# Optimization experiments

Measured on AMD Instinct MI355X. Metric: run time of the kernel, lower is better.

Reference implementation:

```python
import jax, jax.numpy as jnp
import numpy as np

N = 4096  # output_size
B = 4096  # batch rows
NEG_SLOPE = 0.02


def setup_inputs() -> dict:
    key = jax.random.key(0)
    k1, k2, k3, k4 = jax.random.split(key, 4)
    x = jax.random.normal(k1, (B, N), dtype=jnp.float32)
    W = jax.random.normal(k2, (N, N), dtype=jnp.float32)        # self.weights
    beta = jax.random.normal(k3, (1,), dtype=jnp.float32)       # self.beta (scalar param)
    beta_res = jax.random.normal(k4, (N,), dtype=jnp.float32)   # self.res.beta
    return {"x": x, "W": W, "beta": beta, "beta_res": beta_res}


def reference(x, W, beta, beta_res):
    # wrho = x.unsqueeze(1) * W.expand(B,-1,-1); row_sum = wrho.sum(2)  ==  x @ W.T
    row_sum = jnp.einsum("bj,ij->bi", x, W)                 # [B, N]
    out = jax.nn.relu(1.0 - beta + row_sum)                 # hlogic(1 - beta + row_sum)
    # ResEventually: relu(1 - (beta_res - (x + out))), then LeakyReLU(0.02)
    res = jax.nn.relu(1.0 - (beta_res - (x + out)))
    return jnp.where(res >= 0, res, NEG_SLOPE * res)
```

## Files before the change

### kernel.cpp

```cpp
#include <hip/hip_runtime.h>


#define NDIM 4096

typedef __bf16 bf16x8 __attribute__((ext_vector_type(8)));
typedef float f32x4 __attribute__((ext_vector_type(4)));

__device__ unsigned short f2bf(float f) {
    unsigned int x;
    __builtin_memcpy(&x, &f, 4);
    unsigned int r = x + 0x7FFFu + ((x >> 16) & 1u);
    return (unsigned short)(r >> 16);
}

__device__ unsigned int pack_bf2(float lo, float hi) {
    return (unsigned int)f2bf(lo) | ((unsigned int)f2bf(hi) << 16);
}

__device__ inline void gload16(const uint4* g, unsigned int* l) {
    __builtin_amdgcn_global_load_lds(
        (const __attribute__((address_space(1))) unsigned int*)g,
        (__attribute__((address_space(3))) unsigned int*)l,
        16, 0, 0);
}

__global__ void convert_f32_bf16_kernel(const float* src, unsigned int* dst) {
    const size_t i = ((size_t)blockIdx.x * blockDim.x + threadIdx.x) * 8;
    float4 v0 = *(const float4*)(src + i);
    float4 v1 = *(const float4*)(src + i + 4);
    uint4 u;
    u.x = pack_bf2(v0.x, v0.y);
    u.y = pack_bf2(v0.z, v0.w);
    u.z = pack_bf2(v1.x, v1.y);
    u.w = pack_bf2(v1.z, v1.w);
    *(uint4*)(dst + i / 2) = u;
}

#define BAR()   __builtin_amdgcn_s_barrier()
#define VMCNT(n) asm volatile("s_waitcnt vmcnt(" #n ")" ::: "memory")
#define PRIO(x) __builtin_amdgcn_s_setprio(x)

#define STAGE_A(buf, h, S) do { \
    gload16(Ab4 + (offA[2*(h)]   + (S)*8), &sAU[buf][(2*(h))*2048   + wq]); \
    gload16(Ab4 + (offA[2*(h)+1] + (S)*8), &sAU[buf][(2*(h)+1)*2048 + wq]); \
} while (0)
#define STAGE_B(buf, h, S) do { \
    gload16(Bb4 + (offB[2*(h)]   + (S)*8), &sBU[buf][(2*(h))*2048   + wq]); \
    gload16(Bb4 + (offB[2*(h)+1] + (S)*8), &sBU[buf][(2*(h)+1)*2048 + wq]); \
} while (0)

#define READ_A4(dst, pbuf, mt0) do { \
    _Pragma("unroll") for (int _m = 0; _m < 4; _m++) { \
        dst[_m][0] = (pbuf)[afB + ((mt0) + _m) * 128]; \
        dst[_m][1] = (pbuf)[afB + ((mt0) + _m) * 128 + 64]; } \
} while (0)
#define READ_B2(dst, pbuf, nt0) do { \
    _Pragma("unroll") for (int _n = 0; _n < 2; _n++) { \
        dst[_n][0] = (pbuf)[bfB + ((nt0) + _n) * 128]; \
        dst[_n][1] = (pbuf)[bfB + ((nt0) + _n) * 128 + 64]; } \
} while (0)

#define MM16(afr, bfr, mt0, nt0) do { \
    _Pragma("unroll") for (int _k = 0; _k < 2; _k++) \
    _Pragma("unroll") for (int _m = 0; _m < 4; _m++) \
    _Pragma("unroll") for (int _n = 0; _n < 2; _n++) \
        acc[(mt0)+_m][(nt0)+_n] = __builtin_amdgcn_mfma_f32_16x16x32_bf16( \
            afr[_m][_k], bfr[_n][_k], acc[(mt0)+_m][(nt0)+_n], 0, 0, 0); \
} while (0)

__global__ void __launch_bounds__(512, 2)
ResFCEventuallyLayer_82205674045459_kernel(
    const unsigned int* Xbf, const unsigned int* Wbf,
    const float* X, const float* Bp, const float* Br,
    float* out)
{
    __shared__ __align__(16) unsigned int sAU[2][8192];
    __shared__ __align__(16) unsigned int sBU[2][8192];

    const int t    = threadIdx.x;
    const int lane = t & 63;
    const int wave = t >> 6;
    const int quad = lane >> 4;
    const int l16  = lane & 15;
    const int wm   = wave >> 2;
    const int wn   = wave & 3;
    const int wq   = wave * 256;

    const int bid = blockIdx.x;
    const int swz = ((bid & 7) << 5) | (bid >> 3);
    const int bm0 = (swz >> 4) * 256;
    const int bn0 = (swz & 15) * 256;

    const uint4* Ab4 = (const uint4*)Xbf;
    const uint4* Bb4 = (const uint4*)Wbf;

    int offA[4], offB[4];
#pragma unroll
    for (int rr = 0; rr < 4; rr++) {
        const int p   = rr * 512 + t;
        const int r   = (p >> 2) & 15;
        const int sub = p >> 6;
        const int sr  = sub >> 1, sc = sub & 1;
        const int c8  = (p & 3) ^ (((r >> 3) & 1) << 1);
        const int row = sr * 16 + r;
        const int gc  = sc * 4 + c8;
        offA[rr] = (bm0 + row) * 512 + gc;
        offB[rr] = (bn0 + row) * 512 + gc;
    }

    const int laneByte = l16 * 64 + ((quad * 16) ^ (((l16 >> 3) & 1) << 5));
    const int afB = (wm * 16384 + laneByte) >> 4;
    const int bfB = (wn * 8192  + laneByte) >> 4;

    const bf16x8* pA0 = (const bf16x8*)sAU[0];
    const bf16x8* pA1 = (const bf16x8*)sAU[1];
    const bf16x8* pB0 = (const bf16x8*)sBU[0];
    const bf16x8* pB1 = (const bf16x8*)sBU[1];

    f32x4 acc[8][4];
#pragma unroll
    for (int i = 0; i < 8; i++)
#pragma unroll
        for (int j = 0; j < 4; j++)
#pragma unroll
            for (int r = 0; r < 4; r++)
                acc[i][j][r] = 0.0f;

    bf16x8 af0[4][2], af1[4][2], bf0[2][2], bf1[2][2];

    STAGE_A(0, 0, 0); STAGE_B(0, 0, 0); STAGE_B(0, 1, 0); STAGE_A(0, 1, 0);
    STAGE_A(1, 0, 1); STAGE_B(1, 0, 1); STAGE_B(1, 1, 1);
    VMCNT(6);
    BAR();

    for (int j = 0; j < 32; j++) {
        const int S1 = 2 * j + 1;
        const int S2 = (2 * j + 2) & 63;
        const int S3 = (2 * j + 3) & 63;

        STAGE_A(1, 1, S1);
        READ_A4(af0, pA0, 0); READ_B2(bf0, pB0, 0);
        PRIO(1); MM16(af0, bf0, 0, 0); PRIO(0);
        BAR();
        READ_B2(bf1, pB0, 2);
        PRIO(1); MM16(af0, bf1, 0, 2); PRIO(0);
        BAR();
        STAGE_B(0, 0, S2);
        READ_A4(af1, pA0, 4);
        PRIO(1); MM16(af1, bf1, 4, 2); PRIO(0);
        BAR();
        STAGE_B(0, 1, S2);
        STAGE_A(0, 0, S2);
        PRIO(1); MM16(af1, bf0, 4, 0); PRIO(0);
        VMCNT(6);
        BAR();

        STAGE_A(0, 1, S2);
        READ_A4(af0, pA1, 0); READ_B2(bf0, pB1, 0);
        PRIO(1); MM16(af0, bf0, 0, 0); PRIO(0);
        BAR();
        READ_B2(bf1, pB1, 2);
        PRIO(1); MM16(af0, bf1, 0, 2); PRIO(0);
        BAR();
        STAGE_B(1, 0, S3);
        READ_A4(af1, pA1, 4);
        PRIO(1); MM16(af1, bf1, 4, 2); PRIO(0);
        BAR();
        STAGE_B(1, 1, S3);
        STAGE_A(1, 0, S3);
        PRIO(1); MM16(af1, bf0, 4, 0); PRIO(0);
        VMCNT(6);
        BAR();
    }

    const float one_m_beta = 1.0f - Bp[0];
#pragma unroll
    for (int nt = 0; nt < 4; nt++) {
        const int n = bn0 + wn * 64 + nt * 16 + l16;
        const float br = Br[n];
#pragma unroll
        for (int mt = 0; mt < 8; mt++) {
            const int mbase = bm0 + wm * 128 + mt * 16 + quad * 4;
#pragma unroll
            for (int r = 0; r < 4; r++) {
                const size_t idx = (size_t)(mbase + r) * NDIM + n;
                float v = acc[mt][nt][r] + one_m_beta;
                if (v < 0.0f) v = 0.0f;
                float res = 1.0f - br + X[idx] + v;
                if (res < 0.0f) res = 0.0f;
                out[idx] = res;
            }
        }
    }
}

__global__ void resfc_fallback_kernel(
    const float* X, const float* W,
    const float* Bp, const float* Br,
    float* out)
{
    __shared__ __align__(16) unsigned int sA[128 * 16];
    __shared__ __align__(16) unsigned int sB[128 * 16];

    const int t    = threadIdx.x;
    const int lane = t & 63;
    const int wave = t >> 6;
    const int quad = lane >> 4;
    const int l16  = lane & 15;
    const int wm   = wave >> 1;
    const int wn   = wave & 1;

    const int bm0 = blockIdx.y * 128;
    const int bn0 = blockIdx.x * 128;

    const float* gA[4];
    const float* gB[4];
    int ldsIdx[4];
    for (int c = 0; c < 4; c++) {
        const int ch   = t + c * 256;
        const int row  = ch >> 3;
        const int col4 = ch & 7;
        gA[c] = X + (size_t)(bm0 + row) * NDIM + col4 * 4;
        gB[c] = W + (size_t)(bn0 + row) * NDIM + col4 * 4;
        ldsIdx[c] = row * 16 + col4 * 2;
    }

    typedef __bf16 bf16x8_ __attribute__((ext_vector_type(8)));
    const bf16x8* pa = (const bf16x8*)sA + (wm * 64 + l16) * 4 + quad;
    const bf16x8* pb = (const bf16x8*)sB + (wn * 64 + l16) * 4 + quad;

    f32x4 acc[4][4];
    for (int i = 0; i < 4; i++)
        for (int j = 0; j < 4; j++)
            for (int r = 0; r < 4; r++)
                acc[i][j][r] = 0.0f;

    for (int k0 = 0; k0 < NDIM; k0 += 32) {
        float4 va[4], vb[4];
        for (int c = 0; c < 4; c++) {
            va[c] = *(const float4*)(gA[c] + k0);
            vb[c] = *(const float4*)(gB[c] + k0);
        }
        __syncthreads();
        for (int c = 0; c < 4; c++) {
            uint2 ua, ub;
            ua.x = pack_bf2(va[c].x, va[c].y);
            ua.y = pack_bf2(va[c].z, va[c].w);
            ub.x = pack_bf2(vb[c].x, vb[c].y);
            ub.y = pack_bf2(vb[c].z, vb[c].w);
            *(uint2*)(sA + ldsIdx[c]) = ua;
            *(uint2*)(sB + ldsIdx[c]) = ub;
        }
        __syncthreads();

        bf16x8 af[4], bfr[4];
        for (int mt = 0; mt < 4; mt++) af[mt]  = pa[mt * 64];
        for (int nt = 0; nt < 4; nt++) bfr[nt] = pb[nt * 64];

        for (int mt = 0; mt < 4; mt++)
            for (int nt = 0; nt < 4; nt++)
                acc[mt][nt] = __builtin_amdgcn_mfma_f32_16x16x32_bf16(
                    af[mt], bfr[nt], acc[mt][nt], 0, 0, 0);
    }

    const float one_m_beta = 1.0f - Bp[0];
    for (int nt = 0; nt < 4; nt++) {
        const int n = bn0 + wn * 64 + nt * 16 + l16;
        const float br = Br[n];
        for (int mt = 0; mt < 4; mt++) {
            const int mbase = bm0 + wm * 64 + mt * 16 + quad * 4;
            for (int r = 0; r < 4; r++) {
                const size_t idx = (size_t)(mbase + r) * NDIM + n;
                float v = acc[mt][nt][r] + one_m_beta;
                if (v < 0.0f) v = 0.0f;
                float res = 1.0f - br + X[idx] + v;
                if (res < 0.0f) res = 0.0f;
                out[idx] = res;
            }
        }
    }
}

extern "C" void kernel_launch(void* const* d_in, const int* in_sizes, int n_in,
                              void* d_out, int out_size, void* d_ws, size_t ws_size,
                              hipStream_t stream) {
    (void)in_sizes; (void)n_in; (void)out_size;

    const float* X  = (const float*)d_in[0];
    const float* W  = (const float*)d_in[1];
    const float* Bp = (const float*)d_in[2];
    const float* Br = (const float*)d_in[3];
    float* out      = (float*)d_out;

    const size_t elems   = (size_t)NDIM * NDIM;
    const size_t bf_need = elems * 2 * 2;

    dim3 block(256);

    if (ws_size >= bf_need) {
        unsigned int* Xbf = (unsigned int*)d_ws;
        unsigned int* Wbf = (unsigned int*)d_ws + elems / 2;

        dim3 cvt_grid((unsigned int)(elems / 8 / 256));
        hipLaunchKernelGGL(convert_f32_bf16_kernel, cvt_grid, block, 0, stream, X, Xbf);
        hipLaunchKernelGGL(convert_f32_bf16_kernel, cvt_grid, block, 0, stream, W, Wbf);
        hipLaunchKernelGGL(ResFCEventuallyLayer_82205674045459_kernel,
                           dim3(256), dim3(512), 0, stream, Xbf, Wbf, X, Bp, Br, out);
    } else {
        hipLaunchKernelGGL(resfc_fallback_kernel,
                           dim3(NDIM / 128, NDIM / 128), block, 0, stream,
                           X, W, Bp, Br, out);
    }
}
```

Measured before the change: 318.5 us.

## Restructure GEMM main loop pipeline and merge the two bf16 conversion launches

The double-buffered MFMA main loop is reordered so LDS fragment reads for the next sub-tile are issued ahead of the MFMAs that use the current fragments, and each buffer's global->LDS staging is issued as a single block per half-iteration. The per-half barrier count falls from four to two, with a full vmcnt(0) wait before each barrier, so the prefetch depth shrinks somewhat in exchange for less synchronisation and better LDS-read/MFMA overlap. The two fp32->bf16 conversion kernels are also merged into one launch that covers both X and W, removing one kernel launch.

```diff
diff --git a/kernel.cpp b/kernel.cpp
--- a/kernel.cpp
+++ b/kernel.cpp
@@ -24,8 +24,14 @@
         16, 0, 0);
 }
 
-__global__ void convert_f32_bf16_kernel(const float* src, unsigned int* dst) {
-    const size_t i = ((size_t)blockIdx.x * blockDim.x + threadIdx.x) * 8;
+__global__ void convert_f32_bf16_kernel(const float* X, unsigned int* Xbf,
+                                        const float* W, unsigned int* Wbf) {
+    unsigned int bid = blockIdx.x;
+    const float* src;
+    unsigned int* dst;
+    if (bid < 8192) { src = X; dst = Xbf; }
+    else            { src = W; dst = Wbf; bid -= 8192; }
+    const size_t i = ((size_t)bid * blockDim.x + threadIdx.x) * 8;
     float4 v0 = *(const float4*)(src + i);
     float4 v1 = *(const float4*)(src + i + 4);
     uint4 u;
@@ -47,6 +53,10 @@
 #define STAGE_B(buf, h, S) do { \
     gload16(Bb4 + (offB[2*(h)]   + (S)*8), &sBU[buf][(2*(h))*2048   + wq]); \
     gload16(Bb4 + (offB[2*(h)+1] + (S)*8), &sBU[buf][(2*(h)+1)*2048 + wq]); \
+} while (0)
+#define STAGE_ALL(buf, S) do { \
+    STAGE_A(buf, 0, S); STAGE_A(buf, 1, S); \
+    STAGE_B(buf, 0, S); STAGE_B(buf, 1, S); \
 } while (0)
 
 #define READ_A4(dst, pbuf, mt0) do { \
@@ -128,50 +138,42 @@
 
     bf16x8 af0[4][2], af1[4][2], bf0[2][2], bf1[2][2];
 
-    STAGE_A(0, 0, 0); STAGE_B(0, 0, 0); STAGE_B(0, 1, 0); STAGE_A(0, 1, 0);
-    STAGE_A(1, 0, 1); STAGE_B(1, 0, 1); STAGE_B(1, 1, 1);
-    VMCNT(6);
+    STAGE_ALL(0, 0);
+    STAGE_ALL(1, 1);
+    VMCNT(8);
     BAR();
+    READ_B2(bf0, pB0, 0);
+    READ_A4(af1, pA0, 4);
 
     for (int j = 0; j < 32; j++) {
-        const int S1 = 2 * j + 1;
         const int S2 = (2 * j + 2) & 63;
         const int S3 = (2 * j + 3) & 63;
 
-        STAGE_A(1, 1, S1);
-        READ_A4(af0, pA0, 0); READ_B2(bf0, pB0, 0);
+        READ_A4(af0, pA0, 0);
+        PRIO(1); MM16(af1, bf0, 4, 0); PRIO(0);
+        READ_B2(bf1, pB0, 2);
         PRIO(1); MM16(af0, bf0, 0, 0); PRIO(0);
-        BAR();
-        READ_B2(bf1, pB0, 2);
+        VMCNT(0); BAR();
+        READ_B2(bf0, pB1, 0);
         PRIO(1); MM16(af0, bf1, 0, 2); PRIO(0);
         BAR();
-        STAGE_B(0, 0, S2);
-        READ_A4(af1, pA0, 4);
+        READ_A4(af0, pA1, 0);
+        STAGE_ALL(0, S2);
+        PRIO(1); MM16(af1, bf1, 4, 2); PRIO(0);
+
+        READ_A4(af1, pA1, 4);
+        PRIO(1); MM16(af0, bf0, 0, 0); PRIO(0);
+        READ_B2(bf1, pB1, 2);
+        PRIO(1); MM16(af1, bf0, 4, 0); PRIO(0);
+        VMCNT(0); BAR();
+        READ_B2(bf0, pB0, 0);
         PRIO(1); MM16(af1, bf1, 4, 2); PRIO(0);
         BAR();
-        STAGE_B(0, 1, S2);
-        STAGE_A(0, 0, S2);
-        PRIO(1); MM16(af1, bf0, 4, 0); PRIO(0);
-        VMCNT(6);
-        BAR();
-
-        STAGE_A(0, 1, S2);
-        READ_A4(af0, pA1, 0); READ_B2(bf0, pB1, 0);
-        PRIO(1); MM16(af0, bf0, 0, 0); PRIO(0);
-        BAR();
-        READ_B2(bf1, pB1, 2);
+        READ_A4(af1, pA0, 4);
+        STAGE_ALL(1, S3);
         PRIO(1); MM16(af0, bf1, 0, 2); PRIO(0);
-        BAR();
-        STAGE_B(1, 0, S3);
-        READ_A4(af1, pA1, 4);
-        PRIO(1); MM16(af1, bf1, 4, 2); PRIO(0);
-        BAR();
-        STAGE_B(1, 1, S3);
-        STAGE_A(1, 0, S3);
-        PRIO(1); MM16(af1, bf0, 4, 0); PRIO(0);
-        VMCNT(6);
-        BAR();
-    }
+    }
+    VMCNT(0);
 
     const float one_m_beta = 1.0f - Bp[0];
 #pragma unroll
@@ -225,7 +227,6 @@
         ldsIdx[c] = row * 16 + col4 * 2;
     }
 
-    typedef __bf16 bf16x8_ __attribute__((ext_vector_type(8)));
     const bf16x8* pa = (const bf16x8*)sA + (wm * 64 + l16) * 4 + quad;
     const bf16x8* pb = (const bf16x8*)sB + (wn * 64 + l16) * 4 + quad;
 
@@ -295,20 +296,17 @@
     const size_t elems   = (size_t)NDIM * NDIM;
     const size_t bf_need = elems * 2 * 2;
 
-    dim3 block(256);
-
     if (ws_size >= bf_need) {
         unsigned int* Xbf = (unsigned int*)d_ws;
         unsigned int* Wbf = (unsigned int*)d_ws + elems / 2;
 
-        dim3 cvt_grid((unsigned int)(elems / 8 / 256));
-        hipLaunchKernelGGL(convert_f32_bf16_kernel, cvt_grid, block, 0, stream, X, Xbf);
-        hipLaunchKernelGGL(convert_f32_bf16_kernel, cvt_grid, block, 0, stream, W, Wbf);
+        hipLaunchKernelGGL(convert_f32_bf16_kernel, dim3(16384), dim3(256),
+                           0, stream, X, Xbf, W, Wbf);
         hipLaunchKernelGGL(ResFCEventuallyLayer_82205674045459_kernel,
                            dim3(256), dim3(512), 0, stream, Xbf, Wbf, X, Bp, Br, out);
     } else {
         hipLaunchKernelGGL(resfc_fallback_kernel,
-                           dim3(NDIM / 128, NDIM / 128), block, 0, stream,
+                           dim3(NDIM / 128, NDIM / 128), dim3(256), 0, stream,
                            X, W, Bp, Br, out);
     }
 }
```

Measured after the change: 326.8 us. 1.03x slower.

## Fuse fp32-to-bf16 conversion into GEMM staging, drop separate convert kernels

Applied to the files above, without the earlier changes.

Removes the two standalone conversion kernels and the bf16 workspace copies of X and W. The main GEMM kernel now reads fp32 directly from global memory, converts to bf16 in registers, and writes to LDS with ordinary stores instead of async global_load_lds. This saves the extra conversion passes and kernel launches. In exchange, each tile load moves twice the bytes, the loads become synchronous register round-trips that can stall the software pipeline, and barriers become full __syncthreads. The fallback path is also removed.

```diff
diff --git a/kernel.cpp b/kernel.cpp
--- a/kernel.cpp
+++ b/kernel.cpp
@@ -6,48 +6,24 @@
 typedef __bf16 bf16x8 __attribute__((ext_vector_type(8)));
 typedef float f32x4 __attribute__((ext_vector_type(4)));
 
-__device__ unsigned short f2bf(float f) {
-    unsigned int x;
-    __builtin_memcpy(&x, &f, 4);
-    unsigned int r = x + 0x7FFFu + ((x >> 16) & 1u);
-    return (unsigned short)(r >> 16);
-}
-
-__device__ unsigned int pack_bf2(float lo, float hi) {
-    return (unsigned int)f2bf(lo) | ((unsigned int)f2bf(hi) << 16);
-}
-
-__device__ inline void gload16(const uint4* g, unsigned int* l) {
-    __builtin_amdgcn_global_load_lds(
-        (const __attribute__((address_space(1))) unsigned int*)g,
-        (__attribute__((address_space(3))) unsigned int*)l,
-        16, 0, 0);
-}
-
-__global__ void convert_f32_bf16_kernel(const float* src, unsigned int* dst) {
-    const size_t i = ((size_t)blockIdx.x * blockDim.x + threadIdx.x) * 8;
-    float4 v0 = *(const float4*)(src + i);
-    float4 v1 = *(const float4*)(src + i + 4);
-    uint4 u;
-    u.x = pack_bf2(v0.x, v0.y);
-    u.y = pack_bf2(v0.z, v0.w);
-    u.z = pack_bf2(v1.x, v1.y);
-    u.w = pack_bf2(v1.z, v1.w);
-    *(uint4*)(dst + i / 2) = u;
-}
-
-#define BAR()   __builtin_amdgcn_s_barrier()
-#define VMCNT(n) asm volatile("s_waitcnt vmcnt(" #n ")" ::: "memory")
 #define PRIO(x) __builtin_amdgcn_s_setprio(x)
 
-#define STAGE_A(buf, h, S) do { \
-    gload16(Ab4 + (offA[2*(h)]   + (S)*8), &sAU[buf][(2*(h))*2048   + wq]); \
-    gload16(Ab4 + (offA[2*(h)+1] + (S)*8), &sAU[buf][(2*(h)+1)*2048 + wq]); \
+#define CHUNK(sbuf, src, offs, bufi, h, S) do { \
+    _Pragma("unroll") for (int _c = 0; _c < 2; _c++) { \
+        const int _rr = 2 * (h) + _c; \
+        const float4* _g = (const float4*)((src) + offs[_rr] + (size_t)(S) * 64); \
+        const float4 _a = _g[0], _b = _g[1]; \
+        bf16x8 _v; \
+        _v[0] = (__bf16)_a.x; _v[1] = (__bf16)_a.y; \
+        _v[2] = (__bf16)_a.z; _v[3] = (__bf16)_a.w; \
+        _v[4] = (__bf16)_b.x; _v[5] = (__bf16)_b.y; \
+        _v[6] = (__bf16)_b.z; _v[7] = (__bf16)_b.w; \
+        *(bf16x8*)&sbuf[bufi][_rr * 2048 + tq] = _v; \
+    } \
 } while (0)
-#define STAGE_B(buf, h, S) do { \
-    gload16(Bb4 + (offB[2*(h)]   + (S)*8), &sBU[buf][(2*(h))*2048   + wq]); \
-    gload16(Bb4 + (offB[2*(h)+1] + (S)*8), &sBU[buf][(2*(h)+1)*2048 + wq]); \
-} while (0)
+
+#define CHUNK_A(buf, h, S) CHUNK(sAU, X, offA32, buf, h, S)
+#define CHUNK_B(buf, h, S) CHUNK(sBU, W, offB32, buf, h, S)
 
 #define READ_A4(dst, pbuf, mt0) do { \
     _Pragma("unroll") for (int _m = 0; _m < 4; _m++) { \
@@ -70,8 +46,8 @@
 
 __global__ void __launch_bounds__(512, 2)
 ResFCEventuallyLayer_82205674045459_kernel(
-    const unsigned int* Xbf, const unsigned int* Wbf,
-    const float* X, const float* Bp, const float* Br,
+    const float* X, const float* W,
+    const float* Bp, const float* Br,
     float* out)
 {
     __shared__ __align__(16) unsigned int sAU[2][8192];
@@ -84,17 +60,14 @@
     const int l16  = lane & 15;
     const int wm   = wave >> 2;
     const int wn   = wave & 3;
-    const int wq   = wave * 256;
+    const int tq   = t * 4;
 
     const int bid = blockIdx.x;
     const int swz = ((bid & 7) << 5) | (bid >> 3);
     const int bm0 = (swz >> 4) * 256;
     const int bn0 = (swz & 15) * 256;
 
-    const uint4* Ab4 = (const uint4*)Xbf;
-    const uint4* Bb4 = (const uint4*)Wbf;
-
-    int offA[4], offB[4];
+    size_t offA32[4], offB32[4];
 #pragma unroll
     for (int rr = 0; rr < 4; rr++) {
         const int p   = rr * 512 + t;
@@ -104,8 +77,8 @@
         const int c8  = (p & 3) ^ (((r >> 3) & 1) << 1);
         const int row = sr * 16 + r;
         const int gc  = sc * 4 + c8;
-        offA[rr] = (bm0 + row) * 512 + gc;
-        offB[rr] = (bn0 + row) * 512 + gc;
+        offA32[rr] = (size_t)(bm0 + row) * NDIM + gc * 8;
+        offB32[rr] = (size_t)(bn0 + row) * NDIM + gc * 8;
     }
 
     const int laneByte = l16 * 64 + ((quad * 16) ^ (((l16 >> 3) & 1) << 5));
@@ -128,49 +101,46 @@
 
     bf16x8 af0[4][2], af1[4][2], bf0[2][2], bf1[2][2];
 
-    STAGE_A(0, 0, 0); STAGE_B(0, 0, 0); STAGE_B(0, 1, 0); STAGE_A(0, 1, 0);
-    STAGE_A(1, 0, 1); STAGE_B(1, 0, 1); STAGE_B(1, 1, 1);
-    VMCNT(6);
-    BAR();
+    CHUNK_A(0, 0, 0); CHUNK_A(0, 1, 0); CHUNK_B(0, 0, 0); CHUNK_B(0, 1, 0);
+    CHUNK_A(1, 0, 1); CHUNK_A(1, 1, 1); CHUNK_B(1, 0, 1); CHUNK_B(1, 1, 1);
+    __syncthreads();
 
     for (int j = 0; j < 32; j++) {
         const int S1 = 2 * j + 1;
         const int S2 = (2 * j + 2) & 63;
         const int S3 = (2 * j + 3) & 63;
 
-        STAGE_A(1, 1, S1);
+        CHUNK_A(1, 1, S1);
         READ_A4(af0, pA0, 0); READ_B2(bf0, pB0, 0);
         PRIO(1); MM16(af0, bf0, 0, 0); PRIO(0);
-        BAR();
+        __syncthreads();
         READ_B2(bf1, pB0, 2);
         PRIO(1); MM16(af0, bf1, 0, 2); PRIO(0);
-        BAR();
-        STAGE_B(0, 0, S2);
+        __syncthreads();
+        CHUNK_B(0, 0, S2);
         READ_A4(af1, pA0, 4);
         PRIO(1); MM16(af1, bf1, 4, 2); PRIO(0);
-        BAR();
-        STAGE_B(0, 1, S2);
-        STAGE_A(0, 0, S2);
+        __syncthreads();
+        CHUNK_B(0, 1, S2);
+        CHUNK_A(0, 0, S2);
         PRIO(1); MM16(af1, bf0, 4, 0); PRIO(0);
-        VMCNT(6);
-        BAR();
+        __syncthreads();
 
-        STAGE_A(0, 1, S2);
+        CHUNK_A(0, 1, S2);
         READ_A4(af0, pA1, 0); READ_B2(bf0, pB1, 0);
         PRIO(1); MM16(af0, bf0, 0, 0); PRIO(0);
-        BAR();
+        __syncthreads();
         READ_B2(bf1, pB1, 2);
         PRIO(1); MM16(af0, bf1, 0, 2); PRIO(0);
-        BAR();
-        STAGE_B(1, 0, S3);
+        __syncthreads();
+        CHUNK_B(1, 0, S3);
         READ_A4(af1, pA1, 4);
         PRIO(1); MM16(af1, bf1, 4, 2); PRIO(0);
-        BAR();
-        STAGE_B(1, 1, S3);
-        STAGE_A(1, 0, S3);
+        __syncthreads();
+        CHUNK_B(1, 1, S3);
+        CHUNK_A(1, 0, S3);
         PRIO(1); MM16(af1, bf0, 4, 0); PRIO(0);
-        VMCNT(6);
-        BAR();
+        __syncthreads();
     }
 
     const float one_m_beta = 1.0f - Bp[0];
@@ -194,97 +164,10 @@
     }
 }
 
-__global__ void resfc_fallback_kernel(
-    const float* X, const float* W,
-    const float* Bp, const float* Br,
-    float* out)
-{
-    __shared__ __align__(16) unsigned int sA[128 * 16];
-    __shared__ __align__(16) unsigned int sB[128 * 16];
-
-    const int t    = threadIdx.x;
-    const int lane = t & 63;
-    const int wave = t >> 6;
-    const int quad = lane >> 4;
-    const int l16  = lane & 15;
-    const int wm   = wave >> 1;
-    const int wn   = wave & 1;
-
-    const int bm0 = blockIdx.y * 128;
-    const int bn0 = blockIdx.x * 128;
-
-    const float* gA[4];
-    const float* gB[4];
-    int ldsIdx[4];
-    for (int c = 0; c < 4; c++) {
-        const int ch   = t + c * 256;
-        const int row  = ch >> 3;
-        const int col4 = ch & 7;
-        gA[c] = X + (size_t)(bm0 + row) * NDIM + col4 * 4;
-        gB[c] = W + (size_t)(bn0 + row) * NDIM + col4 * 4;
-        ldsIdx[c] = row * 16 + col4 * 2;
-    }
-
-    typedef __bf16 bf16x8_ __attribute__((ext_vector_type(8)));
-    const bf16x8* pa = (const bf16x8*)sA + (wm * 64 + l16) * 4 + quad;
-    const bf16x8* pb = (const bf16x8*)sB + (wn * 64 + l16) * 4 + quad;
-
-    f32x4 acc[4][4];
-    for (int i = 0; i < 4; i++)
-        for (int j = 0; j < 4; j++)
-            for (int r = 0; r < 4; r++)
-                acc[i][j][r] = 0.0f;
-
-    for (int k0 = 0; k0 < NDIM; k0 += 32) {
-        float4 va[4], vb[4];
-        for (int c = 0; c < 4; c++) {
-            va[c] = *(const float4*)(gA[c] + k0);
-            vb[c] = *(const float4*)(gB[c] + k0);
-        }
-        __syncthreads();
-        for (int c = 0; c < 4; c++) {
-            uint2 ua, ub;
-            ua.x = pack_bf2(va[c].x, va[c].y);
-            ua.y = pack_bf2(va[c].z, va[c].w);
-            ub.x = pack_bf2(vb[c].x, vb[c].y);
-            ub.y = pack_bf2(vb[c].z, vb[c].w);
-            *(uint2*)(sA + ldsIdx[c]) = ua;
-            *(uint2*)(sB + ldsIdx[c]) = ub;
-        }
-        __syncthreads();
-
-        bf16x8 af[4], bfr[4];
-        for (int mt = 0; mt < 4; mt++) af[mt]  = pa[mt * 64];
-        for (int nt = 0; nt < 4; nt++) bfr[nt] = pb[nt * 64];
-
-        for (int mt = 0; mt < 4; mt++)
-            for (int nt = 0; nt < 4; nt++)
-                acc[mt][nt] = __builtin_amdgcn_mfma_f32_16x16x32_bf16(
-                    af[mt], bfr[nt], acc[mt][nt], 0, 0, 0);
-    }
-
-    const float one_m_beta = 1.0f - Bp[0];
-    for (int nt = 0; nt < 4; nt++) {
-        const int n = bn0 + wn * 64 + nt * 16 + l16;
-        const float br = Br[n];
-        for (int mt = 0; mt < 4; mt++) {
-            const int mbase = bm0 + wm * 64 + mt * 16 + quad * 4;
-            for (int r = 0; r < 4; r++) {
-                const size_t idx = (size_t)(mbase + r) * NDIM + n;
-                float v = acc[mt][nt][r] + one_m_beta;
-                if (v < 0.0f) v = 0.0f;
-                float res = 1.0f - br + X[idx] + v;
-                if (res < 0.0f) res = 0.0f;
-                out[idx] = res;
-            }
-        }
-    }
-}
-
 extern "C" void kernel_launch(void* const* d_in, const int* in_sizes, int n_in,
                               void* d_out, int out_size, void* d_ws, size_t ws_size,
                               hipStream_t stream) {
-    (void)in_sizes; (void)n_in; (void)out_size;
+    (void)in_sizes; (void)n_in; (void)out_size; (void)d_ws; (void)ws_size;
 
     const float* X  = (const float*)d_in[0];
     const float* W  = (const float*)d_in[1];
@@ -292,23 +175,6 @@
     const float* Br = (const float*)d_in[3];
     float* out      = (float*)d_out;
 
-    const size_t elems   = (size_t)NDIM * NDIM;
-    const size_t bf_need = elems * 2 * 2;
-
-    dim3 block(256);
-
-    if (ws_size >= bf_need) {
-        unsigned int* Xbf = (unsigned int*)d_ws;
-        unsigned int* Wbf = (unsigned int*)d_ws + elems / 2;
-
-        dim3 cvt_grid((unsigned int)(elems / 8 / 256));
-        hipLaunchKernelGGL(convert_f32_bf16_kernel, cvt_grid, block, 0, stream, X, Xbf);
-        hipLaunchKernelGGL(convert_f32_bf16_kernel, cvt_grid, block, 0, stream, W, Wbf);
-        hipLaunchKernelGGL(ResFCEventuallyLayer_82205674045459_kernel,
-                           dim3(256), dim3(512), 0, stream, Xbf, Wbf, X, Bp, Br, out);
-    } else {
-        hipLaunchKernelGGL(resfc_fallback_kernel,
-                           dim3(NDIM / 128, NDIM / 128), block, 0, stream,
-                           X, W, Bp, Br, out);
-    }
+    hipLaunchKernelGGL(ResFCEventuallyLayer_82205674045459_kernel,
+                       dim3(256), dim3(512), 0, stream, X, W, Bp, Br, out);
 }
```

Measured after the change: 452.1 us. +42.0%, slower.

## Merge bf16 conversions into one launch and reshuffle GEMM load staging

Applied to the files above, without the earlier changes.

The two f32-to-bf16 conversion launches are merged into a single kernel that picks X or W by block index, saving one launch and its tail. In the main GEMM loop the global-to-LDS loads are split into single-row issues and spread differently across the barrier phases. A-tile loads are interleaved as rows 0/2 and 1/3, and B-tile loads are spread more evenly between MFMA sections, so load issue overlaps better with compute. The vmcnt wait counts stay the same, so correctness depends on the new issue order still completing each buffer before it is read.

```diff
diff --git a/kernel.cpp b/kernel.cpp
--- a/kernel.cpp
+++ b/kernel.cpp
@@ -24,8 +24,14 @@
         16, 0, 0);
 }
 
-__global__ void convert_f32_bf16_kernel(const float* src, unsigned int* dst) {
-    const size_t i = ((size_t)blockIdx.x * blockDim.x + threadIdx.x) * 8;
+__global__ void convert_f32_bf16_kernel(const float* X, unsigned int* Xbf,
+                                        const float* W, unsigned int* Wbf) {
+    unsigned int bid = blockIdx.x;
+    const float* src;
+    unsigned int* dst;
+    if (bid < 8192) { src = X; dst = Xbf; }
+    else            { src = W; dst = Wbf; bid -= 8192; }
+    const size_t i = ((size_t)bid * blockDim.x + threadIdx.x) * 8;
     float4 v0 = *(const float4*)(src + i);
     float4 v1 = *(const float4*)(src + i + 4);
     uint4 u;
@@ -40,14 +46,10 @@
 #define VMCNT(n) asm volatile("s_waitcnt vmcnt(" #n ")" ::: "memory")
 #define PRIO(x) __builtin_amdgcn_s_setprio(x)
 
-#define STAGE_A(buf, h, S) do { \
-    gload16(Ab4 + (offA[2*(h)]   + (S)*8), &sAU[buf][(2*(h))*2048   + wq]); \
-    gload16(Ab4 + (offA[2*(h)+1] + (S)*8), &sAU[buf][(2*(h)+1)*2048 + wq]); \
-} while (0)
-#define STAGE_B(buf, h, S) do { \
-    gload16(Bb4 + (offB[2*(h)]   + (S)*8), &sBU[buf][(2*(h))*2048   + wq]); \
-    gload16(Bb4 + (offB[2*(h)+1] + (S)*8), &sBU[buf][(2*(h)+1)*2048 + wq]); \
-} while (0)
+#define STAGE1_A(buf, rr, S) \
+    gload16(Ab4 + (offA[rr] + (S) * 8), &sAU[buf][(rr) * 2048 + wq])
+#define STAGE1_B(buf, rr, S) \
+    gload16(Bb4 + (offB[rr] + (S) * 8), &sBU[buf][(rr) * 2048 + wq])
 
 #define READ_A4(dst, pbuf, mt0) do { \
     _Pragma("unroll") for (int _m = 0; _m < 4; _m++) { \
@@ -128,8 +130,10 @@
 
     bf16x8 af0[4][2], af1[4][2], bf0[2][2], bf1[2][2];
 
-    STAGE_A(0, 0, 0); STAGE_B(0, 0, 0); STAGE_B(0, 1, 0); STAGE_A(0, 1, 0);
-    STAGE_A(1, 0, 1); STAGE_B(1, 0, 1); STAGE_B(1, 1, 1);
+    STAGE1_A(0, 0, 0); STAGE1_A(0, 1, 0); STAGE1_A(0, 2, 0); STAGE1_A(0, 3, 0);
+    STAGE1_B(0, 0, 0); STAGE1_B(0, 1, 0); STAGE1_B(0, 2, 0); STAGE1_B(0, 3, 0);
+    STAGE1_B(1, 0, 1); STAGE1_B(1, 1, 1); STAGE1_B(1, 2, 1); STAGE1_B(1, 3, 1);
+    STAGE1_A(1, 0, 1); STAGE1_A(1, 2, 1);
     VMCNT(6);
     BAR();
 
@@ -138,36 +142,36 @@
         const int S2 = (2 * j + 2) & 63;
         const int S3 = (2 * j + 3) & 63;
 
-        STAGE_A(1, 1, S1);
+        STAGE1_A(1, 1, S1); STAGE1_A(1, 3, S1);
         READ_A4(af0, pA0, 0); READ_B2(bf0, pB0, 0);
         PRIO(1); MM16(af0, bf0, 0, 0); PRIO(0);
         BAR();
+        STAGE1_A(0, 0, S2); STAGE1_A(0, 2, S2);
         READ_B2(bf1, pB0, 2);
         PRIO(1); MM16(af0, bf1, 0, 2); PRIO(0);
         BAR();
-        STAGE_B(0, 0, S2);
+        STAGE1_B(0, 0, S2); STAGE1_B(0, 1, S2);
         READ_A4(af1, pA0, 4);
         PRIO(1); MM16(af1, bf1, 4, 2); PRIO(0);
         BAR();
-        STAGE_B(0, 1, S2);
-        STAGE_A(0, 0, S2);
+        STAGE1_B(0, 2, S2); STAGE1_B(0, 3, S2);
         PRIO(1); MM16(af1, bf0, 4, 0); PRIO(0);
         VMCNT(6);
         BAR();
 
-        STAGE_A(0, 1, S2);
+        STAGE1_A(0, 1, S2); STAGE1_A(0, 3, S2);
         READ_A4(af0, pA1, 0); READ_B2(bf0, pB1, 0);
         PRIO(1); MM16(af0, bf0, 0, 0); PRIO(0);
         BAR();
         READ_B2(bf1, pB1, 2);
         PRIO(1); MM16(af0, bf1, 0, 2); PRIO(0);
         BAR();
-        STAGE_B(1, 0, S3);
+        STAGE1_B(1, 0, S3); STAGE1_B(1, 1, S3);
+        STAGE1_B(1, 2, S3); STAGE1_B(1, 3, S3);
         READ_A4(af1, pA1, 4);
         PRIO(1); MM16(af1, bf1, 4, 2); PRIO(0);
         BAR();
-        STAGE_B(1, 1, S3);
-        STAGE_A(1, 0, S3);
+        STAGE1_A(1, 0, S3); STAGE1_A(1, 2, S3);
         PRIO(1); MM16(af1, bf0, 4, 0); PRIO(0);
         VMCNT(6);
         BAR();
@@ -225,7 +229,6 @@
         ldsIdx[c] = row * 16 + col4 * 2;
     }
 
-    typedef __bf16 bf16x8_ __attribute__((ext_vector_type(8)));
     const bf16x8* pa = (const bf16x8*)sA + (wm * 64 + l16) * 4 + quad;
     const bf16x8* pb = (const bf16x8*)sB + (wn * 64 + l16) * 4 + quad;
 
@@ -295,20 +298,17 @@
     const size_t elems   = (size_t)NDIM * NDIM;
     const size_t bf_need = elems * 2 * 2;
 
-    dim3 block(256);
-
     if (ws_size >= bf_need) {
         unsigned int* Xbf = (unsigned int*)d_ws;
         unsigned int* Wbf = (unsigned int*)d_ws + elems / 2;
 
-        dim3 cvt_grid((unsigned int)(elems / 8 / 256));
-        hipLaunchKernelGGL(convert_f32_bf16_kernel, cvt_grid, block, 0, stream, X, Xbf);
-        hipLaunchKernelGGL(convert_f32_bf16_kernel, cvt_grid, block, 0, stream, W, Wbf);
+        hipLaunchKernelGGL(convert_f32_bf16_kernel, dim3(16384), dim3(256),
+                           0, stream, X, Xbf, W, Wbf);
         hipLaunchKernelGGL(ResFCEventuallyLayer_82205674045459_kernel,
                            dim3(256), dim3(512), 0, stream, Xbf, Wbf, X, Bp, Br, out);
     } else {
         hipLaunchKernelGGL(resfc_fallback_kernel,
-                           dim3(NDIM / 128, NDIM / 128), block, 0, stream,
+                           dim3(NDIM / 128, NDIM / 128), dim3(256), 0, stream,
                            X, W, Bp, Br, out);
     }
 }
```

New measurement: 327.5 us. 2.9% more time.
